# Performance work log

Measured on AMD Instinct MI355X. Metric: run time of the kernel, lower is better.

The kernel has to match this reference:

```python
import jax, jax.numpy as jnp
import numpy as np

B, N = 1, 1024
C_A, C_Z, H = 768, 128, 16
CH = C_A // H  # 48
INV_SQRT_CH = float(1.0 / np.sqrt(CH))


def _ln(x, w, b):
    # torch.nn.LayerNorm over last dim, eps=1e-5
    m = jnp.mean(x, axis=-1, keepdims=True)
    v = jnp.mean(jnp.square(x - m), axis=-1, keepdims=True)
    return (x - m) * jax.lax.rsqrt(v + 1e-5) * w + b


def setup_inputs() -> dict:
    key = jax.random.key(0)
    ks = jax.random.split(key, 8)
    rn = lambda k, shape, sc: jax.random.normal(k, shape, dtype=jnp.float32) * sc
    return {
        "a": rn(ks[0], (B, N, C_A), 1.0),
        "z": rn(ks[1], (B, N, N, C_Z), 1.0),
        "mask": jnp.ones((B, N), dtype=jnp.float32),
        "ln_a_w": jnp.ones((C_A,), jnp.float32),
        "ln_a_b": jnp.zeros((C_A,), jnp.float32),
        "ln_z_w": jnp.ones((C_Z,), jnp.float32),
        "ln_z_b": jnp.zeros((C_Z,), jnp.float32),
        "Wq": rn(ks[2], (C_A, H * CH), 0.02),
        "bq": jnp.zeros((H * CH,), jnp.float32),
        "Wk": rn(ks[3], (C_A, H * CH), 0.02),
        "Wv": rn(ks[4], (C_A, H * CH), 0.02),
        "Wb": rn(ks[5], (C_Z, H), 0.02),
        "Wg": rn(ks[6], (C_A, H * CH), 0.02),
        "Wo": rn(ks[7], (H * CH, C_A), 0.02),
    }


def reference(a, z, mask, ln_a_w, ln_a_b, ln_z_w, ln_z_b, Wq, bq, Wk, Wv, Wb, Wg, Wo):
    an = _ln(a, ln_a_w, ln_a_b)                                  # [B, N, C_A]
    q = (an @ Wq + bq).reshape(B, N, H, CH)
    k = (an @ Wk).reshape(B, N, H, CH)
    v = (an @ Wv).reshape(B, N, H, CH)
    # pair bias: LayerNorm(z) -> per-head scalar bias [B, N, N, H]
    bpair = _ln(z, ln_z_w, ln_z_b) @ Wb
    mbias = (mask - 1.0)[:, None, None, :] * 1e9                  # [B, 1, 1, N]
    logits = jnp.einsum('bqhc,bkhc->bhqk', q, k) * INV_SQRT_CH
    logits = logits + jnp.transpose(bpair, (0, 3, 1, 2)) + mbias  # [B, H, N, N]
    attn = jax.nn.softmax(logits, axis=-1)
    o = jnp.einsum('bhqk,bkhc->bqhc', attn, v)                    # [B, N, H, CH]
    g = jax.nn.sigmoid(an @ Wg).reshape(B, N, H, CH)
    out = (g * o).reshape(B, N, H * CH) @ Wo                      # [B, N, C_A]
    return out
```

## Files before the change

kernel.cpp:

```cpp
#include <hip/hip_runtime.h>

#define NSEQ 1024
#define CA   768
#define CZ   128
#define NH   16
#define CHD  48
#define HC   768
#define INV_SQRT_CH 0.14433756729740643f

typedef float v4f __attribute__((ext_vector_type(4)));
typedef short v8s __attribute__((ext_vector_type(8)));

__device__ __forceinline__ short f2bf(float f) {
  union { float f; unsigned u; } v; v.f = f;
  unsigned r = v.u + 0x7fffu + ((v.u >> 16) & 1u);
  return (short)(r >> 16);
}
__device__ __forceinline__ float bf2f(short s) {
  union { unsigned u; float f; } v;
  v.u = ((unsigned)(unsigned short)s) << 16;
  return v.f;
}
__device__ __forceinline__ unsigned cvtpk(float lo, float hi) {
  unsigned r;
  asm("v_cvt_pk_bf16_f32 %0, %1, %2" : "=v"(r) : "v"(lo), "v"(hi));
  return r;
}

__global__ __launch_bounds__(256) void k_front(
    const float* __restrict__ lnzw, const float* __restrict__ lnzb,
    const float* __restrict__ Wb, short* __restrict__ wWp, float* __restrict__ S1bW,
    const float* __restrict__ Wq, const float* __restrict__ Wk,
    const float* __restrict__ Wv, const float* __restrict__ Wg,
    const float* __restrict__ Wo, short* __restrict__ WT, short* __restrict__ WoT,
    const float* __restrict__ a, const float* __restrict__ lnaw,
    const float* __restrict__ lnab, short* __restrict__ anb)
{
  __shared__ __align__(16) char fsm[64 * 65 * 4];
  const int bid = blockIdx.x;
  const int t = threadIdx.x;

  if (bid == 0) {
    const int s = t >> 6, l = t & 63;
    const int r16 = l & 15, cg = l >> 4;
    float v[8];
    #pragma unroll
    for (int j = 0; j < 8; ++j) {
      int d = s * 32 + cg * 8 + j;
      v[j] = lnzw[d] * Wb[d * NH + r16];
    }
    uint4 pk;
    pk.x = cvtpk(v[0], v[1]); pk.y = cvtpk(v[2], v[3]);
    pk.z = cvtpk(v[4], v[5]); pk.w = cvtpk(v[6], v[7]);
    *(uint4*)(wWp + (s * 64 + l) * 8) = pk;
    if (t < NH) {
      float s1 = 0.f, bw = 0.f;
      for (int d = 0; d < CZ; ++d) {
        float wb = Wb[d * NH + t];
        s1 += bf2f(f2bf(lnzw[d] * wb));
        bw += lnzb[d] * wb;
      }
      S1bW[t] = s1;
      S1bW[NH + t] = bw;
    }
  } else if (bid <= 720) {
    float (*tile)[65] = (float(*)[65])fsm;
    const int cb = bid - 1;
    const int mat = cb / 144, rem = cb % 144;
    const int tk = rem % 12, tn = rem / 12;
    const int k0 = tk * 64, n0 = tn * 64;
    const float* __restrict__ W =
        (mat == 0) ? Wq : (mat == 1) ? Wk : (mat == 2) ? Wv : (mat == 3) ? Wg : Wo;
    const float s = (mat == 0) ? INV_SQRT_CH : 1.f;
    const int rr = t >> 4, cc = (t & 15) * 4;
    #pragma unroll
    for (int r = 0; r < 4; ++r) {
      v4f v = *(const v4f*)(W + (size_t)(k0 + r * 16 + rr) * HC + n0 + cc);
      tile[r * 16 + rr][cc + 0] = v[0];
      tile[r * 16 + rr][cc + 1] = v[1];
      tile[r * 16 + rr][cc + 2] = v[2];
      tile[r * 16 + rr][cc + 3] = v[3];
    }
    __syncthreads();
    short* dst = (mat < 4) ? (WT + (size_t)mat * HC * CA) : WoT;
    #pragma unroll
    for (int r = 0; r < 4; ++r) {
      const int nr = r * 16 + rr;
      uint2 pk;
      pk.x = cvtpk(tile[cc + 0][nr] * s, tile[cc + 1][nr] * s);
      pk.y = cvtpk(tile[cc + 2][nr] * s, tile[cc + 3][nr] * s);
      *(uint2*)(dst + (size_t)(n0 + nr) * CA + k0 + cc) = pk;
    }
  } else {
    float* red = (float*)fsm;
    const int row = bid - 721;
    const float* ar = a + (size_t)row * CA;
    float x[3];
    float s = 0.f, s2 = 0.f;
    #pragma unroll
    for (int i = 0; i < 3; ++i) {
      x[i] = ar[t + i * 256];
      s += x[i]; s2 += x[i] * x[i];
    }
    #pragma unroll
    for (int off = 1; off < 64; off <<= 1) {
      s += __shfl_xor(s, off);
      s2 += __shfl_xor(s2, off);
    }
    const int wv = t >> 6;
    if ((t & 63) == 0) { red[wv] = s; red[4 + wv] = s2; }
    __syncthreads();
    s = red[0] + red[1] + red[2] + red[3];
    s2 = red[4] + red[5] + red[6] + red[7];
    const float m = s * (1.f / CA);
    const float var = s2 * (1.f / CA) - m * m;
    const float rs = rsqrtf(var + 1e-5f);
    #pragma unroll
    for (int i = 0; i < 3; ++i) {
      int c = t + i * 256;
      anb[(size_t)row * CA + c] = f2bf((x[i] - m) * rs * lnaw[c] + lnab[c]);
    }
  }
}

__global__ __launch_bounds__(256) void k2_gemm(
    const short* __restrict__ anb, const short* __restrict__ WT,
    const float* __restrict__ bq,
    short* __restrict__ qb, short* __restrict__ kb, short* __restrict__ vT,
    float* __restrict__ gbuf)
{
  __shared__ __align__(16) short As[128 * 40];
  __shared__ __align__(16) short Bs[128 * 40];
  const int tid = threadIdx.x;
  const int w = tid >> 6, l = tid & 63;
  const int r16 = l & 15, cg = l >> 4;
  const int bm = blockIdx.x & 7;
  const int bnb = blockIdx.x >> 3;
  const int m0 = bm * 128, n0 = bnb * 128;
  const int wr = w >> 1, wc = w & 1;
  const int strow = w * 16 + (l >> 2);
  const int scol = (l & 3) * 8;

  v4f acc[4][4];
  #pragma unroll
  for (int i = 0; i < 4; ++i)
    #pragma unroll
    for (int j = 0; j < 4; ++j)
      acc[i][j] = (v4f){0.f, 0.f, 0.f, 0.f};

  for (int k0 = 0; k0 < CA; k0 += 32) {
    v8s av0 = *(const v8s*)(anb + (size_t)(m0 + strow) * CA + k0 + scol);
    v8s av1 = *(const v8s*)(anb + (size_t)(m0 + 64 + strow) * CA + k0 + scol);
    v8s bv0 = *(const v8s*)(WT + (size_t)(n0 + strow) * CA + k0 + scol);
    v8s bv1 = *(const v8s*)(WT + (size_t)(n0 + 64 + strow) * CA + k0 + scol);
    __syncthreads();
    *(v8s*)(As + (size_t)strow * 40 + scol) = av0;
    *(v8s*)(As + (size_t)(64 + strow) * 40 + scol) = av1;
    *(v8s*)(Bs + (size_t)strow * 40 + scol) = bv0;
    *(v8s*)(Bs + (size_t)(64 + strow) * 40 + scol) = bv1;
    __syncthreads();
    v8s a[4], b[4];
    #pragma unroll
    for (int m = 0; m < 4; ++m)
      a[m] = *(const v8s*)(As + (wr * 64 + m * 16 + r16) * 40 + cg * 8);
    #pragma unroll
    for (int n = 0; n < 4; ++n)
      b[n] = *(const v8s*)(Bs + (wc * 64 + n * 16 + r16) * 40 + cg * 8);
    #pragma unroll
    for (int m = 0; m < 4; ++m)
      #pragma unroll
      for (int n = 0; n < 4; ++n)
        acc[m][n] = __builtin_amdgcn_mfma_f32_16x16x32_bf16(a[m], b[n], acc[m][n], 0, 0, 0);
  }

  const int matsel = n0 / HC;
  #pragma unroll
  for (int n = 0; n < 4; ++n) {
    const int nc = (n0 % HC) + wc * 64 + n * 16 + r16;
    const int rbase = m0 + wr * 64 + cg * 4;
    if (matsel == 0) {
      const float bqs = bq[nc] * INV_SQRT_CH;
      #pragma unroll
      for (int m = 0; m < 4; ++m)
        #pragma unroll
        for (int j = 0; j < 4; ++j)
          qb[(size_t)(rbase + m * 16 + j) * HC + nc] = f2bf(acc[m][n][j] + bqs);
    } else if (matsel == 1) {
      #pragma unroll
      for (int m = 0; m < 4; ++m)
        #pragma unroll
        for (int j = 0; j < 4; ++j)
          kb[(size_t)(rbase + m * 16 + j) * HC + nc] = f2bf(acc[m][n][j]);
    } else if (matsel == 2) {
      #pragma unroll
      for (int m = 0; m < 4; ++m) {
        uint2 pk;
        pk.x = cvtpk(acc[m][n][0], acc[m][n][1]);
        pk.y = cvtpk(acc[m][n][2], acc[m][n][3]);
        *(uint2*)(vT + (size_t)nc * NSEQ + rbase + m * 16) = pk;
      }
    } else {
      #pragma unroll
      for (int m = 0; m < 4; ++m)
        #pragma unroll
        for (int j = 0; j < 4; ++j)
          gbuf[(size_t)(rbase + m * 16 + j) * HC + nc] =
              1.f / (1.f + __expf(-acc[m][n][j]));
    }
  }
}

__global__ __launch_bounds__(256) void k3_z(
    const float* __restrict__ z, const short* __restrict__ wWp,
    const float* __restrict__ S1bW, short* __restrict__ bpair)
{
  __shared__ __align__(16) short blds[16 * 72];
  const int tid = threadIdx.x;
  const int w = tid >> 6, l = tid & 63;
  const int r16 = l & 15, cg = l >> 4;
  const int q = blockIdx.x >> 2;
  const int kq = (blockIdx.x & 3) << 8;

  v8s bfrag[4];
  #pragma unroll
  for (int s = 0; s < 4; ++s) bfrag[s] = *(const v8s*)(wWp + (s * 64 + l) * 8);
  const float S1 = S1bW[r16];
  const float bW = S1bW[NH + r16];
  const int h = tid >> 4, kk = (tid & 15) << 2;

  for (int kt = 0; kt < 4; ++kt) {
    const int k0 = kq + kt * 64;
    const int krow = k0 + w * 16 + r16;
    const float* __restrict__ zr = z + ((size_t)q * NSEQ + krow) * CZ;
    float sum = 0.f, sum2 = 0.f;
    v8s afrag[4];
    #pragma unroll
    for (int s = 0; s < 4; ++s) {
      v4f z0 = *(const v4f*)(zr + s * 32 + cg * 8);
      v4f z1 = *(const v4f*)(zr + s * 32 + cg * 8 + 4);
      #pragma unroll
      for (int j = 0; j < 4; ++j) {
        sum += z0[j] + z1[j];
        sum2 += z0[j] * z0[j] + z1[j] * z1[j];
      }
      union { v8s s8; unsigned u[4]; } fu;
      fu.u[0] = cvtpk(z0[0], z0[1]);
      fu.u[1] = cvtpk(z0[2], z0[3]);
      fu.u[2] = cvtpk(z1[0], z1[1]);
      fu.u[3] = cvtpk(z1[2], z1[3]);
      afrag[s] = fu.s8;
    }
    sum  += __shfl_xor(sum, 16);  sum  += __shfl_xor(sum, 32);
    sum2 += __shfl_xor(sum2, 16); sum2 += __shfl_xor(sum2, 32);
    const float mean = sum * (1.f / CZ);
    const float var = sum2 * (1.f / CZ) - mean * mean;
    const float rs = rsqrtf(var + 1e-5f);

    v4f acc = {0.f, 0.f, 0.f, 0.f};
    #pragma unroll
    for (int s = 0; s < 4; ++s)
      acc = __builtin_amdgcn_mfma_f32_16x16x32_bf16(afrag[s], bfrag[s], acc, 0, 0, 0);

    float bv[4];
    #pragma unroll
    for (int j = 0; j < 4; ++j) {
      int src = cg * 4 + j;
      float mj = __shfl(mean, src);
      float rj = __shfl(rs, src);
      bv[j] = rj * (acc[j] - mj * S1) + bW;
    }
    uint2 bu;
    bu.x = cvtpk(bv[0], bv[1]);
    bu.y = cvtpk(bv[2], bv[3]);
    *(uint2*)&blds[r16 * 72 + w * 16 + cg * 4] = bu;
    __syncthreads();
    uint2 v = *(const uint2*)&blds[h * 72 + kk];
    *(uint2*)(bpair + (size_t)h * NSEQ * NSEQ + (size_t)q * NSEQ + k0 + kk) = v;
    __syncthreads();
  }
}

#define PL_STRIDE 136
#define PO_STRIDE 52
__global__ __launch_bounds__(512) void k45_attn(
    const short* __restrict__ qb, const short* __restrict__ kb,
    const short* __restrict__ vT, const short* __restrict__ bpair,
    const float* __restrict__ mask, const float* __restrict__ gbuf,
    short* __restrict__ gob)
{
  const int h = blockIdx.x & 15;
  const int qt = blockIdx.x >> 4;
  const int tid = threadIdx.x;
  const int w = tid >> 6, l = tid & 63;
  const int r16 = l & 15, cg = l >> 4;
  const int q0 = qt * 16;
  const int k0 = w * 128;

  __shared__ __align__(16) short plds[8][16 * PL_STRIDE];
  __shared__ __align__(16) float po_lds[8][16][PO_STRIDE];
  __shared__ __align__(16) float ml_lds[8][16][2];
  short* pl = &plds[w][0];

  const v8s vzero = {0, 0, 0, 0, 0, 0, 0, 0};
  v8s qf0, qf1;
  {
    const short* qp = qb + (size_t)(q0 + r16) * HC + h * CHD;
    qf0 = *(const v8s*)(qp + cg * 8);
    qf1 = (cg < 2) ? *(const v8s*)(qp + 32 + cg * 8) : vzero;
  }

  const size_t bpb = (size_t)h * NSEQ * NSEQ;
  {
    const int srow = l >> 2;
    const int scol = (l & 3) * 32;
    const short* bsrc = bpair + bpb + (size_t)(q0 + srow) * NSEQ + k0 + scol;
    short* bdst = pl + srow * PL_STRIDE + scol;
    v8s t0 = *(const v8s*)(bsrc);
    v8s t1 = *(const v8s*)(bsrc + 8);
    v8s t2 = *(const v8s*)(bsrc + 16);
    v8s t3 = *(const v8s*)(bsrc + 24);
    *(v8s*)(bdst)      = t0;
    *(v8s*)(bdst + 8)  = t1;
    *(v8s*)(bdst + 16) = t2;
    *(v8s*)(bdst + 24) = t3;
  }

  v4f cs[8];
  #pragma unroll
  for (int kt = 0; kt < 8; ++kt) {
    const short* kp = kb + (size_t)(k0 + kt * 16 + r16) * HC + h * CHD;
    v8s b0 = *(const v8s*)(kp + cg * 8);
    v8s b1 = (cg < 2) ? *(const v8s*)(kp + 32 + cg * 8) : vzero;
    v4f tacc = {0.f, 0.f, 0.f, 0.f};
    tacc = __builtin_amdgcn_mfma_f32_16x16x32_bf16(qf0, b0, tacc, 0, 0, 0);
    tacc = __builtin_amdgcn_mfma_f32_16x16x32_bf16(qf1, b1, tacc, 0, 0, 0);
    cs[kt] = tacc;
  }

  #pragma unroll
  for (int kt = 0; kt < 8; ++kt) {
    const int kc = k0 + kt * 16 + r16;
    const float mb = (mask[kc] - 1.f) * 1e9f;
    #pragma unroll
    for (int j = 0; j < 4; ++j)
      cs[kt][j] += bf2f(pl[(cg * 4 + j) * PL_STRIDE + kt * 16 + r16]) + mb;
  }

  float mx4[4], ls4[4];
  #pragma unroll
  for (int j = 0; j < 4; ++j) {
    float mx = fmaxf(fmaxf(fmaxf(cs[0][j], cs[1][j]), fmaxf(cs[2][j], cs[3][j])),
                     fmaxf(fmaxf(cs[4][j], cs[5][j]), fmaxf(cs[6][j], cs[7][j])));
    mx = fmaxf(mx, __shfl_xor(mx, 1));
    mx = fmaxf(mx, __shfl_xor(mx, 2));
    mx = fmaxf(mx, __shfl_xor(mx, 4));
    mx = fmaxf(mx, __shfl_xor(mx, 8));
    mx4[j] = mx;
    float p[8];
    #pragma unroll
    for (int kt = 0; kt < 8; ++kt) p[kt] = __expf(cs[kt][j] - mx);
    float rsum = ((p[0] + p[1]) + (p[2] + p[3])) + ((p[4] + p[5]) + (p[6] + p[7]));
    rsum += __shfl_xor(rsum, 1);
    rsum += __shfl_xor(rsum, 2);
    rsum += __shfl_xor(rsum, 4);
    rsum += __shfl_xor(rsum, 8);
    ls4[j] = rsum;
    const int rowb = (cg * 4 + j) * PL_STRIDE;
    #pragma unroll
    for (int t2 = 0; t2 < 4; ++t2) {
      unsigned u = cvtpk(p[2 * t2], p[2 * t2 + 1]);
      pl[rowb + (2 * t2) * 16 + r16] = (short)u;
      pl[rowb + (2 * t2 + 1) * 16 + r16] = (short)(u >> 16);
    }
  }
  asm volatile("s_waitcnt lgkmcnt(0)" ::: "memory");
  __builtin_amdgcn_sched_barrier(0);

  v4f of0 = {0, 0, 0, 0}, of1 = {0, 0, 0, 0}, of2 = {0, 0, 0, 0};
  #pragma unroll
  for (int ks4 = 0; ks4 < 4; ++ks4) {
    v8s pa = *(const v8s*)(pl + r16 * PL_STRIDE + ks4 * 32 + cg * 8);
    const short* vp = vT + (size_t)(h * CHD + r16) * NSEQ + k0 + ks4 * 32 + cg * 8;
    v8s bv0 = *(const v8s*)vp;
    v8s bv1 = *(const v8s*)(vp + 16 * NSEQ);
    v8s bv2 = *(const v8s*)(vp + 32 * NSEQ);
    of0 = __builtin_amdgcn_mfma_f32_16x16x32_bf16(pa, bv0, of0, 0, 0, 0);
    of1 = __builtin_amdgcn_mfma_f32_16x16x32_bf16(pa, bv1, of1, 0, 0, 0);
    of2 = __builtin_amdgcn_mfma_f32_16x16x32_bf16(pa, bv2, of2, 0, 0, 0);
  }

  #pragma unroll
  for (int j = 0; j < 4; ++j) {
    const int row = cg * 4 + j;
    po_lds[w][row][r16]      = of0[j];
    po_lds[w][row][16 + r16] = of1[j];
    po_lds[w][row][32 + r16] = of2[j];
    if (r16 == 0) {
      ml_lds[w][row][0] = mx4[j];
      ml_lds[w][row][1] = ls4[j];
    }
  }
  __syncthreads();

  {
    const int g = tid >> 5;
    const int lane = tid & 31;
    float mi[8], li[8];
    #pragma unroll
    for (int i = 0; i < 8; ++i) {
      mi[i] = ml_lds[i][g][0];
      li[i] = ml_lds[i][g][1];
    }
    float mstar = -1e30f;
    #pragma unroll
    for (int i = 0; i < 8; ++i) mstar = fmaxf(mstar, mi[i]);
    float wgt[8], L = 0.f;
    #pragma unroll
    for (int i = 0; i < 8; ++i) { wgt[i] = __expf(mi[i] - mstar); L += li[i] * wgt[i]; }
    const float inv = 1.f / L;
    const int q = q0 + g;
    {
      float o = 0.f;
      #pragma unroll
      for (int i = 0; i < 8; ++i) o += po_lds[i][g][lane] * wgt[i];
      const float gv = gbuf[(size_t)q * HC + h * CHD + lane];
      gob[(size_t)q * HC + h * CHD + lane] = f2bf(o * inv * gv);
    }
    if (lane < 16) {
      const int d = 32 + lane;
      float o = 0.f;
      #pragma unroll
      for (int i = 0; i < 8; ++i) o += po_lds[i][g][d] * wgt[i];
      const float gv = gbuf[(size_t)q * HC + h * CHD + d];
      gob[(size_t)q * HC + h * CHD + d] = f2bf(o * inv * gv);
    }
  }
}

__global__ __launch_bounds__(256) void k5_out(
    const short* __restrict__ gob, const short* __restrict__ WoT,
    float* __restrict__ out)
{
  __shared__ __align__(16) short As[64 * 40];
  __shared__ __align__(16) short Bs[64 * 40];
  const int tid = threadIdx.x;
  const int w = tid >> 6, l = tid & 63;
  const int r16 = l & 15, cg = l >> 4;
  const int bm = blockIdx.x & 15;
  const int bn = blockIdx.x >> 4;
  const int m0 = bm * 64, n0 = bn * 64;
  const int wr = w >> 1, wc = w & 1;
  const int strow = tid >> 2;
  const int scol = (tid & 3) * 8;

  v4f acc[2][2];
  #pragma unroll
  for (int i = 0; i < 2; ++i)
    #pragma unroll
    for (int j = 0; j < 2; ++j)
      acc[i][j] = (v4f){0.f, 0.f, 0.f, 0.f};

  for (int k0 = 0; k0 < CA; k0 += 32) {
    v8s av = *(const v8s*)(gob + (size_t)(m0 + strow) * CA + k0 + scol);
    v8s bv = *(const v8s*)(WoT + (size_t)(n0 + strow) * CA + k0 + scol);
    __syncthreads();
    *(v8s*)(As + (size_t)strow * 40 + scol) = av;
    *(v8s*)(Bs + (size_t)strow * 40 + scol) = bv;
    __syncthreads();
    v8s a[2], b[2];
    #pragma unroll
    for (int m = 0; m < 2; ++m)
      a[m] = *(const v8s*)(As + (wr * 32 + m * 16 + r16) * 40 + cg * 8);
    #pragma unroll
    for (int n = 0; n < 2; ++n)
      b[n] = *(const v8s*)(Bs + (wc * 32 + n * 16 + r16) * 40 + cg * 8);
    #pragma unroll
    for (int m = 0; m < 2; ++m)
      #pragma unroll
      for (int n = 0; n < 2; ++n)
        acc[m][n] = __builtin_amdgcn_mfma_f32_16x16x32_bf16(a[m], b[n], acc[m][n], 0, 0, 0);
  }

  #pragma unroll
  for (int n = 0; n < 2; ++n) {
    const int nc = n0 + wc * 32 + n * 16 + r16;
    const int rbase = m0 + wr * 32 + cg * 4;
    #pragma unroll
    for (int m = 0; m < 2; ++m)
      #pragma unroll
      for (int j = 0; j < 4; ++j)
        out[(size_t)(rbase + m * 16 + j) * CA + nc] = acc[m][n][j];
  }
}

extern "C" void kernel_launch(void* const* d_in, const int* in_sizes, int n_in,
                              void* d_out, int out_size, void* d_ws, size_t ws_size,
                              hipStream_t stream) {
  const float* a      = (const float*)d_in[0];
  const float* z      = (const float*)d_in[1];
  const float* mask   = (const float*)d_in[2];
  const float* ln_a_w = (const float*)d_in[3];
  const float* ln_a_b = (const float*)d_in[4];
  const float* ln_z_w = (const float*)d_in[5];
  const float* ln_z_b = (const float*)d_in[6];
  const float* Wq     = (const float*)d_in[7];
  const float* bq     = (const float*)d_in[8];
  const float* Wk     = (const float*)d_in[9];
  const float* Wv     = (const float*)d_in[10];
  const float* Wb     = (const float*)d_in[11];
  const float* Wg     = (const float*)d_in[12];
  const float* Wo     = (const float*)d_in[13];
  float* out = (float*)d_out;

  char* ws = (char*)d_ws;
  short* anb   = (short*)(ws);
  short* WT    = (short*)(ws + (2ull << 20));
  short* WoT   = (short*)(ws + (7ull << 20));
  short* qb    = (short*)(ws + (9ull << 20));
  short* kb    = (short*)(ws + (11ull << 20));
  short* vT    = (short*)(ws + (13ull << 20));
  float* gbuf  = (float*)(ws + (15ull << 20));
  short* wWp   = (short*)(ws + (19ull << 20));
  float* S1bW  = (float*)(ws + (19ull << 20) + 4096ull);
  short* gob   = (short*)(ws + (20ull << 20));
  short* bpair = (short*)(ws + (22ull << 20));

  k_front<<<1745, 256, 0, stream>>>(ln_z_w, ln_z_b, Wb, wWp, S1bW,
                                    Wq, Wk, Wv, Wg, Wo, WT, WoT,
                                    a, ln_a_w, ln_a_b, anb);
  k2_gemm<<<192, 256, 0, stream>>>(anb, WT, bq, qb, kb, vT, gbuf);
  k3_z<<<4096, 256, 0, stream>>>(z, wWp, S1bW, bpair);
  k45_attn<<<1024, 512, 0, stream>>>(qb, kb, vT, bpair, mask, gbuf, gob);
  k5_out<<<192, 256, 0, stream>>>(gob, WoT, out);
}
```

Measured before the change: 194.8 us.

## Pipeline z loads and use per-wave LDS transpose in pair-bias kernel

Each wave of k3_z now owns a contiguous 64-key slice. It prefetches the next 16-row z tile into registers while computing the current one, which hides global-load latency. Each wave keeps a private LDS tile, so the two block-wide __syncthreads per iteration are gone. Bias rows are written once at the end as 32-byte vector stores instead of 8-byte stores. The cost is extra register pressure from the double-buffered z fragments and reliance on an explicit lgkmcnt wait for intra-wave LDS ordering.

```diff
diff --git a/kernel.cpp b/kernel.cpp
--- a/kernel.cpp
+++ b/kernel.cpp
@@ -210,34 +210,50 @@
   }
 }
 
+#define BL_SH 68
 __global__ __launch_bounds__(256) void k3_z(
     const float* __restrict__ z, const short* __restrict__ wWp,
     const float* __restrict__ S1bW, short* __restrict__ bpair)
 {
-  __shared__ __align__(16) short blds[16 * 72];
+  __shared__ __align__(16) short blds[4][16 * BL_SH];
   const int tid = threadIdx.x;
   const int w = tid >> 6, l = tid & 63;
   const int r16 = l & 15, cg = l >> 4;
   const int q = blockIdx.x >> 2;
-  const int kq = (blockIdx.x & 3) << 8;
+  const int kw = ((blockIdx.x & 3) << 8) + w * 64;
+  short* bl = &blds[w][0];
 
   v8s bfrag[4];
   #pragma unroll
   for (int s = 0; s < 4; ++s) bfrag[s] = *(const v8s*)(wWp + (s * 64 + l) * 8);
   const float S1 = S1bW[r16];
   const float bW = S1bW[NH + r16];
-  const int h = tid >> 4, kk = (tid & 15) << 2;
+
+  const float* __restrict__ zbase = z + ((size_t)q * NSEQ + kw + r16) * CZ;
+
+  v4f zb[8];
+  #pragma unroll
+  for (int s = 0; s < 4; ++s) {
+    zb[2 * s]     = *(const v4f*)(zbase + s * 32 + cg * 8);
+    zb[2 * s + 1] = *(const v4f*)(zbase + s * 32 + cg * 8 + 4);
+  }
 
   for (int kt = 0; kt < 4; ++kt) {
-    const int k0 = kq + kt * 64;
-    const int krow = k0 + w * 16 + r16;
-    const float* __restrict__ zr = z + ((size_t)q * NSEQ + krow) * CZ;
+    v4f zn[8];
+    if (kt < 3) {
+      const float* __restrict__ zr2 = zbase + (size_t)(kt + 1) * 16 * CZ;
+      #pragma unroll
+      for (int s = 0; s < 4; ++s) {
+        zn[2 * s]     = *(const v4f*)(zr2 + s * 32 + cg * 8);
+        zn[2 * s + 1] = *(const v4f*)(zr2 + s * 32 + cg * 8 + 4);
+      }
+    }
+
     float sum = 0.f, sum2 = 0.f;
     v8s afrag[4];
     #pragma unroll
     for (int s = 0; s < 4; ++s) {
-      v4f z0 = *(const v4f*)(zr + s * 32 + cg * 8);
-      v4f z1 = *(const v4f*)(zr + s * 32 + cg * 8 + 4);
+      v4f z0 = zb[2 * s], z1 = zb[2 * s + 1];
       #pragma unroll
       for (int j = 0; j < 4; ++j) {
         sum += z0[j] + z1[j];
@@ -269,15 +285,24 @@
       float rj = __shfl(rs, src);
       bv[j] = rj * (acc[j] - mj * S1) + bW;
     }
-    uint2 bu;
-    bu.x = cvtpk(bv[0], bv[1]);
-    bu.y = cvtpk(bv[2], bv[3]);
-    *(uint2*)&blds[r16 * 72 + w * 16 + cg * 4] = bu;
-    __syncthreads();
-    uint2 v = *(const uint2*)&blds[h * 72 + kk];
-    *(uint2*)(bpair + (size_t)h * NSEQ * NSEQ + (size_t)q * NSEQ + k0 + kk) = v;
-    __syncthreads();
-  }
+    *(unsigned*)&bl[r16 * BL_SH + kt * 16 + cg * 4]     = cvtpk(bv[0], bv[1]);
+    *(unsigned*)&bl[r16 * BL_SH + kt * 16 + cg * 4 + 2] = cvtpk(bv[2], bv[3]);
+
+    if (kt < 3) {
+      #pragma unroll
+      for (int i = 0; i < 8; ++i) zb[i] = zn[i];
+    }
+  }
+
+  asm volatile("s_waitcnt lgkmcnt(0)" ::: "memory");
+  __builtin_amdgcn_sched_barrier(0);
+
+  const int h = l >> 2, ck = (l & 3) * 16;
+  v8s o0 = *(const v8s*)(bl + h * BL_SH + ck);
+  v8s o1 = *(const v8s*)(bl + h * BL_SH + ck + 8);
+  short* dst = bpair + (size_t)h * NSEQ * NSEQ + (size_t)q * NSEQ + kw + ck;
+  *(v8s*)(dst)     = o0;
+  *(v8s*)(dst + 8) = o1;
 }
 
 #define PL_STRIDE 136
```

New measurement: 194.7 us. Within noise of the previous version (-0.1%).
